# Kernel optimization log

Hardware: AMD Instinct MI355X
Metric: run time of the kernel (lower is better)

The kernel has to match this reference:

```python
import jax, jax.numpy as jnp
import numpy as np

WS = 14      # window_size
NH = 12      # num_heads


def setup_inputs() -> dict:
    key = jax.random.key(0)
    k0, k1, k2 = jax.random.split(key, 3)
    B, H, W, C = 8, 56, 56, 768
    x = jax.random.normal(k0, (B, H * W, C), jnp.float32)
    s = 1.0 / np.sqrt(C).astype(np.float32)
    w_qkv = jax.random.normal(k1, (C, 3 * C), jnp.float32) * s   # qkv_bias=False
    w_proj = jax.random.normal(k2, (C, C), jnp.float32) * s
    b_proj = jnp.zeros((C,), jnp.float32)
    return {"x": x, "w_qkv": w_qkv, "w_proj": w_proj, "b_proj": b_proj, "H": H, "W": W}


def reference(x, w_qkv, w_proj, b_proj, H, W):
    ws, nh = WS, NH
    B, N, C = x.shape
    hd = C // nh
    H_ = -(-H // ws) * ws
    W_ = -(-W // ws) * ws
    Hn, Wn = H_ // ws, W_ // ws
    L, N_ = Hn * Wn, ws * ws

    qkv = x @ w_qkv                                   # [B, N, 3C]
    qkv = qkv.reshape(B, H, W, 3 * C)
    # pad AFTER the linear, as in the torch code (padded positions have qkv == 0)
    qkv = jnp.pad(qkv, ((0, 0), (0, H_ - H), (0, W_ - W), (0, 0)))
    # window partition: [B,Hn,ws,Wn,ws,3,nh,hd] -> [3,B,L,nh,N_,hd]
    qkv = qkv.reshape(B, Hn, ws, Wn, ws, 3, nh, hd)
    qkv = qkv.transpose(5, 0, 1, 3, 6, 2, 4, 7).reshape(3, B, L, nh, N_, hd)
    q, k, v = qkv[0], qkv[1], qkv[2]

    scale = hd ** -0.5
    attn = jnp.einsum('blhnd,blhmd->blhnm', q * scale, k)   # [B,L,nh,N_,N_]
    attn = jax.nn.softmax(attn, axis=-1)
    out = jnp.einsum('blhnm,blhmd->blhnd', attn, v)          # [B,L,nh,N_,hd]

    # fold windows back: -> [B,H_,W_,C], crop, flatten
    out = out.reshape(B, Hn, Wn, nh, ws, ws, hd)
    out = out.transpose(0, 1, 4, 2, 5, 3, 6).reshape(B, H_, W_, C)
    out = out[:, :H, :W].reshape(B, N, C)
    return out @ w_proj + b_proj
```

## Files before the change

kernel.cpp:

```cpp
#include <hip/hip_runtime.h>

typedef unsigned short u16;
typedef __attribute__((ext_vector_type(8))) __bf16 bf16x8;
typedef __attribute__((ext_vector_type(4))) float floatx4;

__device__ inline float bf2f(u16 u) {
  union { unsigned u; float f; } v; v.u = ((unsigned)u) << 16; return v.f;
}
__device__ inline u16 f2bf(float f) {
  union { float f; unsigned u; } v; v.f = f;
  unsigned r = v.u + 0x7fffu + ((v.u >> 16) & 1u);
  return (u16)(r >> 16);
}

__device__ inline void glds16(const u16* g, u16* l) {
  __builtin_amdgcn_global_load_lds((const __attribute__((address_space(1))) void*)g,
                                   (__attribute__((address_space(3))) void*)l, 16, 0, 0);
}

__global__ __launch_bounds__(256) void detect_k(const u16* __restrict__ w, int* flag)
{
  __shared__ int cnt;
  if (threadIdx.x == 0) cnt = 0;
  __syncthreads();
  int c = 0;
  for (int i = threadIdx.x; i < 16384; i += 256) {
    const int e = (w[i] >> 7) & 0xFF;
    if (e < 64 || e > 191) ++c;
  }
  atomicAdd(&cnt, c);
  __syncthreads();
  if (threadIdx.x == 0) *flag = (cnt > 256) ? 1 : 0;
}

__global__ __launch_bounds__(256) void cast_x_k(const void* __restrict__ in,
                                                u16* __restrict__ out,
                                                int n4, const int* __restrict__ flag)
{
  const int i = blockIdx.x * 256 + threadIdx.x;
  if (i >= n4) return;
  if (*flag) {
    const float4 v = ((const float4*)in)[i];
    u16 o0 = f2bf(v.x), o1 = f2bf(v.y), o2 = f2bf(v.z), o3 = f2bf(v.w);
    uint2 p; p.x = (unsigned)o0 | ((unsigned)o1 << 16); p.y = (unsigned)o2 | ((unsigned)o3 << 16);
    ((uint2*)out)[i] = p;
  } else {
    ((uint2*)out)[i] = ((const uint2*)in)[i];
  }
}

__global__ __launch_bounds__(256) void ct_transpose_k(const void* __restrict__ in,
                                                      u16* __restrict__ out,
                                                      int R, int C, const int* __restrict__ flag)
{
  __shared__ u16 tile[32][33];
  const int f = *flag;
  const int c0 = blockIdx.x * 32, r0 = blockIdx.y * 32;
  const int tx = threadIdx.x & 31, ty = threadIdx.x >> 5;
#pragma unroll
  for (int i = ty; i < 32; i += 8) {
    const size_t idx = (size_t)(r0 + i) * C + (c0 + tx);
    tile[i][tx] = f ? f2bf(((const float*)in)[idx]) : ((const u16*)in)[idx];
  }
  __syncthreads();
#pragma unroll
  for (int i = ty; i < 32; i += 8)
    out[(size_t)(c0 + i) * R + (r0 + tx)] = tile[tx][i];
}

__global__ __launch_bounds__(256) void bias_cast_k(const void* __restrict__ in,
                                                   float* __restrict__ out,
                                                   int n, const int* __restrict__ flag)
{
  const int i = blockIdx.x * 256 + threadIdx.x;
  if (i >= n) return;
  out[i] = *flag ? ((const float*)in)[i] : bf2f(((const u16*)in)[i]);
}

__global__ __launch_bounds__(512) void gemm256(
    const u16* __restrict__ A, const u16* __restrict__ Bt,
    const float* __restrict__ bias, void* __restrict__ C,
    int M, int N, int K, const int* __restrict__ flag, int flagOut)
{
  __shared__ u16 smem[65536];
  const int t = threadIdx.x;
  const int wave = t >> 6, lane = t & 63;
  const int quad = lane >> 4, l15 = lane & 15;
  const int wm = wave >> 2, wn = wave & 3;

  const int nwg = gridDim.x;
  const int q = nwg >> 3, r8 = nwg & 7;
  const int xcd = blockIdx.x & 7, loc = blockIdx.x >> 3;
  const int wg = (xcd < r8 ? xcd * (q + 1) : r8 * (q + 1) + (xcd - r8) * q) + loc;
  const int MT = M >> 8;
  const int mt = wg % MT, ntile = wg / MT;
  const size_t m0 = (size_t)mt << 8;
  const size_t n0 = (size_t)ntile << 8;

  int addrA[8], addrB[4];
#pragma unroll
  for (int i = 0; i < 8; ++i) {
    const int row = wm * 128 + i * 16 + l15;
    const int hs = (((row & 1) << 2) | quad) ^ ((row >> 1) & 7);
    addrA[i] = (row >> 1) * 64 + hs * 8;
  }
#pragma unroll
  for (int j = 0; j < 4; ++j) {
    const int row = wn * 64 + j * 16 + l15;
    const int hs = (((row & 1) << 2) | quad) ^ ((row >> 1) & 7);
    addrB[j] = (row >> 1) * 64 + hs * 8;
  }

  const u16* aSrc[2]; const u16* bSrc[2]; int dstOff[2];
#pragma unroll
  for (int p = 0; p < 2; ++p) {
    const int S = p * 512 + wave * 64 + lane;
    const int line = S >> 3;
    const int h = (S & 7) ^ (line & 7);
    const int row = line * 2 + (h >> 2);
    const int g = (h & 3) * 8;
    aSrc[p] = A + (m0 + row) * (size_t)K + g;
    bSrc[p] = Bt + (n0 + row) * (size_t)K + g;
    dstOff[p] = p * 4096 + wave * 512;
  }

  const int NTk = K >> 5;
  floatx4 acc[8][4] = {};

#pragma unroll
  for (int pt = 0; pt < 3; ++pt) {
#pragma unroll
    for (int p = 0; p < 2; ++p) glds16(aSrc[p] + pt * 32, smem + pt * 8192 + dstOff[p]);
#pragma unroll
    for (int p = 0; p < 2; ++p) glds16(bSrc[p] + pt * 32, smem + 32768 + pt * 8192 + dstOff[p]);
  }
  asm volatile("s_waitcnt vmcnt(8)\n\ts_barrier" ::: "memory");

  for (int kt = 0; kt < NTk; ++kt) {
    const int rb = kt & 3;
    const u16* sA = smem + rb * 8192;
    const u16* sB = smem + 32768 + rb * 8192;

    if (kt + 3 < NTk) {
      const int pre = (kt + 3) * 32;
      const int pr = (kt + 3) & 3;
      glds16(aSrc[0] + pre, smem + pr * 8192 + dstOff[0]);
      glds16(aSrc[1] + pre, smem + pr * 8192 + dstOff[1]);
      glds16(bSrc[0] + pre, smem + 32768 + pr * 8192 + dstOff[0]);
      glds16(bSrc[1] + pre, smem + 32768 + pr * 8192 + dstOff[1]);
    }

    bf16x8 b[4], a[8];
#pragma unroll
    for (int j = 0; j < 4; ++j) b[j] = *(const bf16x8*)(sB + addrB[j]);
#pragma unroll
    for (int i = 0; i < 8; ++i) a[i] = *(const bf16x8*)(sA + addrA[i]);

    __builtin_amdgcn_s_setprio(1);
#pragma unroll
    for (int i = 0; i < 8; ++i)
#pragma unroll
      for (int j = 0; j < 4; ++j)
        acc[i][j] = __builtin_amdgcn_mfma_f32_16x16x32_bf16(a[i], b[j], acc[i][j], 0, 0, 0);
    __builtin_amdgcn_s_setprio(0);

    if (kt < NTk - 3)       asm volatile("s_waitcnt vmcnt(8)\n\ts_barrier" ::: "memory");
    else if (kt == NTk - 3) asm volatile("s_waitcnt vmcnt(4)\n\ts_barrier" ::: "memory");
    else if (kt == NTk - 2) asm volatile("s_waitcnt vmcnt(0)\n\ts_barrier" ::: "memory");
    else                    asm volatile("s_barrier" ::: "memory");
  }

  float bvj[4];
#pragma unroll
  for (int j = 0; j < 4; ++j)
    bvj[j] = bias ? bias[n0 + wn * 64 + j * 16 + l15] : 0.0f;

  if (flagOut && (*flag)) {
    float* scrf = (float*)smem + wave * 1088;
    float* Cf = (float*)C;
#pragma unroll
    for (int i = 0; i < 8; ++i) {
#pragma unroll
      for (int j = 0; j < 4; ++j)
#pragma unroll
        for (int rr = 0; rr < 4; ++rr)
          scrf[(quad * 4 + rr) * 68 + j * 16 + l15] = acc[i][j][rr] + bvj[j];
#pragma unroll
      for (int u = lane; u < 256; u += 64) {
        const int row = u >> 4, gr = u & 15;
        float4 vv = *(const float4*)(scrf + row * 68 + gr * 4);
        *(float4*)(Cf + (m0 + wm * 128 + i * 16 + row) * (size_t)N + n0 + wn * 64 + gr * 4) = vv;
      }
    }
  } else {
    u16* scr = smem + wave * 1152;
    u16* Cb = (u16*)C;
#pragma unroll
    for (int i = 0; i < 8; ++i) {
#pragma unroll
      for (int j = 0; j < 4; ++j)
#pragma unroll
        for (int rr = 0; rr < 4; ++rr)
          scr[(quad * 4 + rr) * 72 + j * 16 + l15] = f2bf(acc[i][j][rr] + bvj[j]);
#pragma unroll
      for (int u = lane; u < 128; u += 64) {
        const int row = u >> 3, gr = u & 7;
        int4 vv = *(const int4*)(scr + row * 72 + gr * 8);
        *(int4*)(Cb + (m0 + wm * 128 + i * 16 + row) * (size_t)N + n0 + wn * 64 + gr * 8) = vv;
      }
    }
  }
}

__global__ __launch_bounds__(256, 2) void attn_win(
    const u16* __restrict__ qkv, u16* __restrict__ o)
{
  __shared__ u16 Ks[196 * 64];
  __shared__ u16 Vt[64 * 208];
  __shared__ u16 Pb[4][16 * 208];
  __shared__ int gtok[208];

  const int bid = blockIdx.x;
  const int h = bid % 12;
  const int l = (bid / 12) % 16;
  const int b = bid / 192;
  const int wr0 = (l >> 2) * 14, wc0 = (l & 3) * 14;
  const int baseTok = b * 3136;

  const int t = threadIdx.x, wave = t >> 6, lane = t & 63;
  const int quad = lane >> 4, l15 = lane & 15;

  if (t < 208) {
    const int nn = t < 196 ? t : 195;
    gtok[t] = baseTok + (wr0 + nn / 14) * 56 + wc0 + nn % 14;
  }
  __syncthreads();

  for (int u = t; u < 196 * 8; u += 256) {
    const int row = u >> 3, gg = u & 7;
    int4 kv = *(const int4*)(qkv + (size_t)gtok[row] * 2304 + 768 + h * 64 + gg * 8);
    *(int4*)(Ks + (row * 8 + (gg ^ (row & 7))) * 8) = kv;
  }
  for (int u = t; u < 208 * 8; u += 256) {
    const int n = u >> 3, dg = u & 7;
    int4 vv = {0, 0, 0, 0};
    if (n < 196)
      vv = *(const int4*)(qkv + (size_t)gtok[n] * 2304 + 1536 + h * 64 + dg * 8);
    const u16* pv = (const u16*)&vv;
#pragma unroll
    for (int j = 0; j < 8; ++j) Vt[(dg * 8 + j) * 208 + n] = pv[j];
  }
  __syncthreads();

  u16* Pw = &Pb[wave][0];
  const bf16x8 zerov = {};

  for (int rt = wave; rt < 13; rt += 4) {
    const int n0r = rt * 16;
    int qn = n0r + l15; if (qn > 195) qn = 195;
    const u16* qrow = qkv + (size_t)gtok[qn] * 2304 + h * 64;
    const bf16x8 aq0 = *(const bf16x8*)(qrow + quad * 8);
    const bf16x8 aq1 = *(const bf16x8*)(qrow + 32 + quad * 8);

    floatx4 s[13];
#pragma unroll
    for (int ct = 0; ct < 13; ++ct) {
      int kr = ct * 16 + l15; if (kr > 195) kr = 195;
      const bf16x8 bk0 = *(const bf16x8*)(Ks + (kr * 8 + (quad ^ (kr & 7))) * 8);
      const bf16x8 bk1 = *(const bf16x8*)(Ks + (kr * 8 + ((quad + 4) ^ (kr & 7))) * 8);
      floatx4 z = {};
      z = __builtin_amdgcn_mfma_f32_16x16x32_bf16(aq0, bk0, z, 0, 0, 0);
      z = __builtin_amdgcn_mfma_f32_16x16x32_bf16(aq1, bk1, z, 0, 0, 0);
      s[ct] = z;
    }

    float mx[4], sm[4];
#pragma unroll
    for (int r = 0; r < 4; ++r) mx[r] = -3e38f;
#pragma unroll
    for (int ct = 0; ct < 13; ++ct) {
      const bool maskct = (ct == 12) && (l15 >= 4);
#pragma unroll
      for (int r = 0; r < 4; ++r) {
        float v = s[ct][r] * 0.125f;
        if (maskct) v = -3e38f;
        s[ct][r] = v;
        mx[r] = fmaxf(mx[r], v);
      }
    }
#pragma unroll
    for (int r = 0; r < 4; ++r)
      for (int off = 1; off < 16; off <<= 1)
        mx[r] = fmaxf(mx[r], __shfl_xor(mx[r], off, 64));
#pragma unroll
    for (int r = 0; r < 4; ++r) sm[r] = 0.0f;
#pragma unroll
    for (int ct = 0; ct < 13; ++ct)
#pragma unroll
      for (int r = 0; r < 4; ++r) {
        const float p = __expf(s[ct][r] - mx[r]);
        s[ct][r] = p;
        sm[r] += p;
      }
#pragma unroll
    for (int r = 0; r < 4; ++r)
      for (int off = 1; off < 16; off <<= 1)
        sm[r] += __shfl_xor(sm[r], off, 64);

#pragma unroll
    for (int ct = 0; ct < 13; ++ct)
#pragma unroll
      for (int r = 0; r < 4; ++r)
        Pw[(quad * 4 + r) * 208 + ct * 16 + l15] = f2bf(s[ct][r]);

    floatx4 oacc[4] = {};
#pragma unroll
    for (int ks = 0; ks < 6; ++ks) {
      const bf16x8 ap = *(const bf16x8*)(Pw + l15 * 208 + ks * 32 + quad * 8);
#pragma unroll
      for (int nt = 0; nt < 4; ++nt) {
        const bf16x8 bv = *(const bf16x8*)(Vt + (nt * 16 + l15) * 208 + ks * 32 + quad * 8);
        oacc[nt] = __builtin_amdgcn_mfma_f32_16x16x32_bf16(ap, bv, oacc[nt], 0, 0, 0);
      }
    }
    {
      const int off = 192 + (quad & 1) * 8;
      bf16x8 ap = *(const bf16x8*)(Pw + l15 * 208 + off);
      if (quad >= 2) ap = zerov;
#pragma unroll
      for (int nt = 0; nt < 4; ++nt) {
        const bf16x8 bv = *(const bf16x8*)(Vt + (nt * 16 + l15) * 208 + off);
        oacc[nt] = __builtin_amdgcn_mfma_f32_16x16x32_bf16(ap, bv, oacc[nt], 0, 0, 0);
      }
    }

    float rs[4];
#pragma unroll
    for (int r = 0; r < 4; ++r) rs[r] = 1.0f / sm[r];

#pragma unroll
    for (int nt = 0; nt < 4; ++nt)
#pragma unroll
      for (int r = 0; r < 4; ++r)
        Pw[(quad * 4 + r) * 208 + nt * 16 + l15] = f2bf(oacc[nt][r] * rs[r]);
#pragma unroll
    for (int u = lane; u < 128; u += 64) {
      const int row = u >> 3, gr = u & 7;
      const int n = n0r + row;
      if (n < 196) {
        int4 vv = *(const int4*)(Pw + row * 208 + gr * 8);
        *(int4*)(o + (size_t)gtok[n] * 768 + h * 64 + gr * 8) = vv;
      }
    }
  }
}

extern "C" void kernel_launch(void* const* d_in, const int* in_sizes, int n_in,
                              void* d_out, int out_size, void* d_ws, size_t ws_size,
                              hipStream_t stream)
{
  const void* x     = d_in[0];
  const void* wqkv  = d_in[1];
  const void* wproj = d_in[2];
  const void* bproj = d_in[3];

  char* ws = (char*)d_ws;
  int*   flag   = (int*)ws;
  float* bprojF = (float*)(ws + 16);
  u16*   wqkvT  = (u16*)(ws + 4096);
  u16*   wprojT = (u16*)(ws + 3543040);
  u16*   qkvbuf = (u16*)(ws + 4722688);
  u16*   xb     = (u16*)(ws + 120328192);
  u16*   attno  = xb;

  detect_k<<<1, 256, 0, stream>>>((const u16*)wqkv, flag);
  cast_x_k<<<dim3(18816), 256, 0, stream>>>(x, xb, 4816896, flag);
  ct_transpose_k<<<dim3(72, 24), 256, 0, stream>>>(wqkv, wqkvT, 768, 2304, flag);
  ct_transpose_k<<<dim3(24, 24), 256, 0, stream>>>(wproj, wprojT, 768, 768, flag);
  bias_cast_k<<<dim3(3), 256, 0, stream>>>(bproj, bprojF, 768, flag);

  gemm256<<<dim3(882), 512, 0, stream>>>(xb, wqkvT, (const float*)nullptr, qkvbuf,
                                         25088, 2304, 768, flag, 0);
  attn_win<<<dim3(1536), 256, 0, stream>>>(qkvbuf, attno);
  gemm256<<<dim3(294), 512, 0, stream>>>(attno, wprojT, bprojF, d_out,
                                         25088, 768, 768, flag, 1);
}
```

Baseline: 395.2 us.

## Split GEMM MFMA phase around barrier and request two workgroups per CU

The 256x256 GEMM main loop now prefetches two k-tiles ahead instead of three. Each iteration is split into two MFMA halves: the barrier and the LDS load of the next B fragments sit between them, so B reads overlap compute. Launch bounds now ask for two 512-thread workgroups per CU to raise occupancy. The cost is a tighter register budget, since the 128-float accumulator alone may approach the cap and cause spills, plus a shallower prefetch that hides less memory latency.

```diff
diff --git a/kernel.cpp b/kernel.cpp
--- a/kernel.cpp
+++ b/kernel.cpp
@@ -77,7 +77,7 @@
   out[i] = *flag ? ((const float*)in)[i] : bf2f(((const u16*)in)[i]);
 }
 
-__global__ __launch_bounds__(512) void gemm256(
+__global__ __launch_bounds__(512, 2) void gemm256(
     const u16* __restrict__ A, const u16* __restrict__ Bt,
     const float* __restrict__ bias, void* __restrict__ C,
     int M, int N, int K, const int* __restrict__ flag, int flagOut)
@@ -128,47 +128,73 @@
   floatx4 acc[8][4] = {};
 
 #pragma unroll
-  for (int pt = 0; pt < 3; ++pt) {
+  for (int pt = 0; pt < 2; ++pt) {
 #pragma unroll
     for (int p = 0; p < 2; ++p) glds16(aSrc[p] + pt * 32, smem + pt * 8192 + dstOff[p]);
 #pragma unroll
     for (int p = 0; p < 2; ++p) glds16(bSrc[p] + pt * 32, smem + 32768 + pt * 8192 + dstOff[p]);
   }
-  asm volatile("s_waitcnt vmcnt(8)\n\ts_barrier" ::: "memory");
+  asm volatile("s_waitcnt vmcnt(4)\n\ts_barrier" ::: "memory");
+
+  bf16x8 bcur[4];
+#pragma unroll
+  for (int j = 0; j < 4; ++j) bcur[j] = *(const bf16x8*)(smem + 32768 + addrB[j]);
 
   for (int kt = 0; kt < NTk; ++kt) {
-    const int rb = kt & 3;
-    const u16* sA = smem + rb * 8192;
-    const u16* sB = smem + 32768 + rb * 8192;
-
-    if (kt + 3 < NTk) {
-      const int pre = (kt + 3) * 32;
-      const int pr = (kt + 3) & 3;
+    const u16* sA = smem + (kt & 3) * 8192;
+
+    if (kt + 2 < NTk) {
+      const int pre = (kt + 2) * 32;
+      const int pr = (kt + 2) & 3;
       glds16(aSrc[0] + pre, smem + pr * 8192 + dstOff[0]);
       glds16(aSrc[1] + pre, smem + pr * 8192 + dstOff[1]);
       glds16(bSrc[0] + pre, smem + 32768 + pr * 8192 + dstOff[0]);
       glds16(bSrc[1] + pre, smem + 32768 + pr * 8192 + dstOff[1]);
     }
 
-    bf16x8 b[4], a[8];
-#pragma unroll
-    for (int j = 0; j < 4; ++j) b[j] = *(const bf16x8*)(sB + addrB[j]);
-#pragma unroll
-    for (int i = 0; i < 8; ++i) a[i] = *(const bf16x8*)(sA + addrA[i]);
+    bf16x8 a03[4], a47[4];
+#pragma unroll
+    for (int i = 0; i < 4; ++i) a03[i] = *(const bf16x8*)(sA + addrA[i]);
+#pragma unroll
+    for (int i = 0; i < 4; ++i) a47[i] = *(const bf16x8*)(sA + addrA[4 + i]);
 
     __builtin_amdgcn_s_setprio(1);
 #pragma unroll
-    for (int i = 0; i < 8; ++i)
+    for (int i = 0; i < 4; ++i)
 #pragma unroll
       for (int j = 0; j < 4; ++j)
-        acc[i][j] = __builtin_amdgcn_mfma_f32_16x16x32_bf16(a[i], b[j], acc[i][j], 0, 0, 0);
+        acc[i][j] = __builtin_amdgcn_mfma_f32_16x16x32_bf16(a03[i], bcur[j], acc[i][j], 0, 0, 0);
     __builtin_amdgcn_s_setprio(0);
 
-    if (kt < NTk - 3)       asm volatile("s_waitcnt vmcnt(8)\n\ts_barrier" ::: "memory");
-    else if (kt == NTk - 3) asm volatile("s_waitcnt vmcnt(4)\n\ts_barrier" ::: "memory");
-    else if (kt == NTk - 2) asm volatile("s_waitcnt vmcnt(0)\n\ts_barrier" ::: "memory");
-    else                    asm volatile("s_barrier" ::: "memory");
-  }
+    if (kt + 1 < NTk) {
+      if (kt + 2 < NTk) asm volatile("s_waitcnt vmcnt(4)\n\ts_barrier" ::: "memory");
+      else              asm volatile("s_waitcnt vmcnt(0)\n\ts_barrier" ::: "memory");
+
+      const u16* sBn = smem + 32768 + ((kt + 1) & 3) * 8192;
+      bf16x8 bn[4];
+#pragma unroll
+      for (int j = 0; j < 4; ++j) bn[j] = *(const bf16x8*)(sBn + addrB[j]);
+
+      __builtin_amdgcn_s_setprio(1);
+#pragma unroll
+      for (int i = 0; i < 4; ++i)
+#pragma unroll
+        for (int j = 0; j < 4; ++j)
+          acc[4 + i][j] = __builtin_amdgcn_mfma_f32_16x16x32_bf16(a47[i], bcur[j], acc[4 + i][j], 0, 0, 0);
+      __builtin_amdgcn_s_setprio(0);
+
+#pragma unroll
+      for (int j = 0; j < 4; ++j) bcur[j] = bn[j];
+    } else {
+#pragma unroll
+      for (int i = 0; i < 4; ++i)
+#pragma unroll
+        for (int j = 0; j < 4; ++j)
+          acc[4 + i][j] = __builtin_amdgcn_mfma_f32_16x16x32_bf16(a47[i], bcur[j], acc[4 + i][j], 0, 0, 0);
+    }
+  }
+
+  __syncthreads();
 
   float bvj[4];
 #pragma unroll
```

Result: no change. 390.8 us (-1.1%).
